# Performance work log

Measured on AMD Instinct MI355X. Metric: run time of the kernel, lower is better.

Reference implementation:

```python
import jax, jax.numpy as jnp
from jax import lax
import numpy as np

EPS = 1e-5

def _conv(x, w, pad):
    return lax.conv_general_dilated(x, w, (1, 1), ((pad, pad), (pad, pad)),
                                    dimension_numbers=('NCHW', 'OIHW', 'NCHW'))

def _bn_relu(x, g, b, m, v):
    scale = g * lax.rsqrt(v + EPS)
    shift = b - m * scale
    return jax.nn.relu(x * scale[:, None, None] + shift[:, None, None])

def _pam(x, kw, kb, vw, vb, gamma):
    # x: [B,C,H,W]; key/query share the same 1x1 conv (as in source)
    B, C, H, W = x.shape
    q = (_conv(x, kw, 0) + kb[:, None, None]).reshape(B, -1, H * W)      # [B,C/8,HW]
    attn = jax.nn.softmax(jnp.einsum('bci,bcj->bij', q, q), axis=-1)     # [B,HW,HW]
    v = (_conv(x, vw, 0) + vb[:, None, None]).reshape(B, C, H * W)       # [B,C,HW]
    out = jnp.einsum('bcj,bij->bci', v, attn).reshape(B, C, H, W)        # value @ attn^T
    return gamma * out + x

def _cam(x, gamma):
    B, C, H, W = x.shape
    f = x.reshape(B, C, H * W)
    energy = jnp.einsum('bcm,bdm->bcd', f, f)                            # [B,C,C]
    attn = jax.nn.softmax(jnp.max(energy, -1, keepdims=True) - energy, axis=-1)
    out = jnp.einsum('bcd,bdm->bcm', attn, f).reshape(B, C, H, W)
    return gamma * out + x

def setup_inputs() -> dict:
    key = jax.random.key(0)
    ks = iter(jax.random.split(key, 40))
    Cin, Cm, Cout = 512, 128, 64  # in_channels, in_channels//ratio, out_channels
    Ck = Cm // 8                  # PAM key channels
    n = lambda shape, s: jax.random.normal(next(ks), shape, jnp.float32) * s
    def bn(c):
        return dict(g=n((c,), 1.0) * 0 + 1.0 + n((c,), 0.1),
                    b=n((c,), 0.1), m=n((c,), 0.1), v=jnp.abs(n((c,), 0.5)) + 0.5)
    bn11, bn12, bn21, bn22 = bn(Cm), bn(Cm), bn(Cm), bn(Cm)
    return {
        'x': jax.random.normal(next(ks), (4, Cin, 64, 64), jnp.float32),
        'w11': n((Cm, Cin, 3, 3), 0.02), 'g11': bn11['g'], 'b11': bn11['b'], 'm11': bn11['m'], 'v11': bn11['v'],
        'w12': n((Cm, Cin, 3, 3), 0.02), 'g12': bn12['g'], 'b12': bn12['b'], 'm12': bn12['m'], 'v12': bn12['v'],
        'pam_kw': n((Ck, Cm, 1, 1), 0.05), 'pam_kb': n((Ck,), 0.02),
        'pam_vw': n((Cm, Cm, 1, 1), 0.05), 'pam_vb': n((Cm,), 0.02),
        'pam_gamma': n((1,), 0.1), 'cam_gamma': n((1,), 0.1),
        'w21': n((Cm, Cm, 3, 3), 0.03), 'g21': bn21['g'], 'b21': bn21['b'], 'm21': bn21['m'], 'v21': bn21['v'],
        'w22': n((Cm, Cm, 3, 3), 0.03), 'g22': bn22['g'], 'b22': bn22['b'], 'm22': bn22['m'], 'v22': bn22['v'],
        'w31': n((Cout, Cm, 1, 1), 0.05), 'b31': n((Cout,), 0.02),
        'w32': n((Cout, Cm, 1, 1), 0.05), 'b32': n((Cout,), 0.02),
        'w4':  n((Cout, Cm, 1, 1), 0.05), 'b4':  n((Cout,), 0.02),
    }

def reference(x, w11, g11, b11, m11, v11, w12, g12, b12, m12, v12,
              pam_kw, pam_kb, pam_vw, pam_vb, pam_gamma, cam_gamma,
              w21, g21, b21, m21, v21, w22, g22, b22, m22, v22,
              w31, b31, w32, b32, w4, b4):
    # Dropout2d(p=0.1) is identity at eval time; BatchNorm uses running stats.
    feat1 = _bn_relu(_conv(x, w11, 1), g11, b11, m11, v11)
    pa_feat = _pam(feat1, pam_kw, pam_kb, pam_vw, pam_vb, pam_gamma)
    pa_conv = _bn_relu(_conv(pa_feat, w21, 1), g21, b21, m21, v21)
    pa_out = _conv(pa_conv, w31, 0) + b31[:, None, None]

    feat2 = _bn_relu(_conv(x, w12, 1), g12, b12, m12, v12)
    ca_feat = _cam(feat2, cam_gamma)
    ca_conv = _bn_relu(_conv(ca_feat, w22, 1), g22, b22, m22, v22)
    ca_out = _conv(ca_conv, w32, 0) + b32[:, None, None]

    feat_sum = pa_conv + ca_conv
    feat_sum_out = _conv(feat_sum, w4, 0) + b4[:, None, None]
    return jnp.stack([pa_out, ca_out, feat_sum_out])  # [3,B,Cout,H,W]
```

## Files before the change

kernel.cpp:

```cpp
#include <hip/hip_runtime.h>
#include <stdint.h>

typedef unsigned short u16;
typedef unsigned int   u32;
typedef unsigned long long u64;
typedef __attribute__((ext_vector_type(8))) short bf16x8;
typedef __attribute__((ext_vector_type(4))) float f32x4;

#define DEV static __device__ __forceinline__

DEV float b2f(u16 u){ u32 x = ((u32)u) << 16; float f; __builtin_memcpy(&f, &x, 4); return f; }
DEV u16 f2b(float f){ u32 x; __builtin_memcpy(&x, &f, 4); return (u16)((x + 0x7fffu + ((x >> 16) & 1u)) >> 16); }
DEV u16 f2b_trunc(float f){ u32 x; __builtin_memcpy(&x, &f, 4); return (u16)(x >> 16); }
DEV float ldf(const void* p, int i, int flg){
  return flg ? b2f(((const u16*)p)[i]) : ((const float*)p)[i];
}
DEV void gload_lds16(const u16* g, u16* l){
  __builtin_amdgcn_global_load_lds((const __attribute__((address_space(1))) void*)g,
                                   (__attribute__((address_space(3))) void*)l, 16, 0, 0);
}

static constexpr int HW   = 4096;
static constexpr int PPIX = 4356;

__global__ void k_prep(
    const u32* __restrict__ x,
    const void* g0,const void* b0,const void* m0,const void* v0,
    const void* g1,const void* b1,const void* m1,const void* v1,
    const void* g2,const void* b2,const void* m2,const void* v2,
    const void* g3,const void* b3,const void* m3,const void* v3,
    int* __restrict__ flag, float* scale, float* shift)
{
  __shared__ int cnt;
  __shared__ int sflag;
  const int t = threadIdx.x;
  if (t == 0) cnt = 0;
  __syncthreads();
  const u32 w  = x[t];
  const u32 eb = (w >> 7) & 0xFFu;
  if (eb >= 100u && eb <= 150u) atomicAdd(&cnt, 1);
  __syncthreads();
  if (t == 0){ sflag = (cnt > 384) ? 1 : 0; *flag = sflag; }
  __syncthreads();
  const int flg = sflag;
  const int set = t >> 7, c = t & 127;
  const void *gp,*bp,*mp,*vp;
  if      (set == 0){gp=g0;bp=b0;mp=m0;vp=v0;}
  else if (set == 1){gp=g1;bp=b1;mp=m1;vp=v1;}
  else if (set == 2){gp=g2;bp=b2;mp=m2;vp=v2;}
  else              {gp=g3;bp=b3;mp=m3;vp=v3;}
  const float sc = ldf(gp,c,flg) * rsqrtf(ldf(vp,c,flg) + 1e-5f);
  scale[t] = sc;
  shift[t] = ldf(bp,c,flg) - ldf(mp,c,flg) * sc;
}

__global__ void k_cvt5(
    const void* s0,const void* s1,const void* s2,const void* s3,const void* s4,
    const int* __restrict__ flagp,
    u16* d0,u16* d1,u16* d2,u16* d3,u16* d4)
{
  const int g = blockIdx.x * 256 + threadIdx.x;
  if (g >= 10752) return;
  const void* s; u16* d; int base;
  if      (g < 512) { s=s0; d=d0; base=0;    }
  else if (g < 4608){ s=s1; d=d1; base=512;  }
  else if (g < 6656){ s=s2; d=d2; base=4608; }
  else if (g < 8704){ s=s3; d=d3; base=6656; }
  else              { s=s4; d=d4; base=8704; }
  const int i = g - base;
  u64 ov;
  if (*flagp){
    ov = ((const u64*)s)[i];
  } else {
    const float4 f = ((const float4*)s)[i];
    const u16 a0 = f2b(f.x), a1 = f2b(f.y), a2 = f2b(f.z), a3 = f2b(f.w);
    ov = (u64)a0 | ((u64)a1 << 16) | ((u64)a2 << 32) | ((u64)a3 << 48);
  }
  ((u64*)d)[i] = ov;
}

__global__ void k_reorder4(
    const void* w11,const void* w12,const void* w21,const void* w22,
    const int* __restrict__ flagp,
    u16* o11,u16* o12,u16* o21,u16* o22)
{
  int blk = blockIdx.x;
  const void* win; u16* wout; int cin;
  if      (blk < 2304){ win=w11; wout=o11; cin=512; }
  else if (blk < 4608){ win=w12; wout=o12; cin=512; blk-=2304; }
  else if (blk < 5184){ win=w21; wout=o21; cin=128; blk-=4608; }
  else                { win=w22; wout=o22; cin=128; blk-=5184; }
  const int idx = blk * 256 + threadIdx.x;
  const int flg = *flagp;
  const int n9 = cin * 9;
  const int co = idx / n9;
  const int rem = idx - co * n9;
  const int ci = rem / 9;
  const int rs = rem - ci * 9;
  const u16 v = flg ? ((const u16*)win)[idx] : f2b(((const float*)win)[idx]);
  wout[co * n9 + rs * cin + ci] = v;
}

__global__ void k_halo3(u16* __restrict__ xT, u16* __restrict__ f1, u16* __restrict__ cf)
{
  int blk = blockIdx.x;
  u16* buf; int cmask, csh;
  if      (blk < 260){ buf = xT; cmask = 511; csh = 9; }
  else if (blk < 325){ buf = f1; cmask = 127; csh = 7; blk -= 260; }
  else               { buf = cf; cmask = 127; csh = 7; blk -= 325; }
  const int tid = blk * 256 + threadIdx.x;
  const int e  = tid * 8;
  const int cc = e & cmask;
  const int rem = e >> csh;
  const int hp = rem % 260;
  const int b  = rem / 260;
  int pix;
  if      (hp < 66)  pix = hp;
  else if (hp < 132) pix = 65 * 66 + (hp - 66);
  else if (hp < 196) pix = (hp - 132 + 1) * 66;
  else               pix = (hp - 196 + 1) * 66 + 65;
  uint4 z; z.x = 0; z.y = 0; z.z = 0; z.w = 0;
  *(uint4*)(buf + ((size_t)b * PPIX + pix) * (cmask + 1) + cc) = z;
}

__global__ __launch_bounds__(256) void k_xT(
    const void* __restrict__ src, const int* __restrict__ flagp, u16* __restrict__ dst)
{
  const int t = threadIdx.x, wave = t >> 6, lane = t & 63;
  const int pb = blockIdx.x & 31, ct = (blockIdx.x >> 5) & 7, b = blockIdx.x >> 8;
  const int c  = ct * 64 + lane;
  const int p0 = pb * 128 + wave * 32;
  const size_t sbase = ((size_t)(b * 512) + c) * 4096 + p0;

  u16 vals[32];
  if (*flagp){
    const u16* s = (const u16*)src + sbase;
    #pragma unroll
    for (int k = 0; k < 4; ++k){
      uint4 v = *(const uint4*)(s + k * 8);
      __builtin_memcpy(&vals[k * 8], &v, 16);
    }
  } else {
    const float* s = (const float*)src + sbase;
    #pragma unroll
    for (int k = 0; k < 8; ++k){
      float4 v = *(const float4*)(s + k * 4);
      vals[k*4+0] = f2b(v.x); vals[k*4+1] = f2b(v.y);
      vals[k*4+2] = f2b(v.z); vals[k*4+3] = f2b(v.w);
    }
  }
  const int hrow = (p0 >> 6) * 66 + (p0 & 63) + 67;
  u16* d = dst + ((size_t)b * PPIX + hrow) * 512 + c;
  #pragma unroll
  for (int k = 0; k < 32; ++k) d[(size_t)k * 512] = vals[k];
}

template<int CIN_, bool PADOUT_, bool DUALB_>
__global__ __launch_bounds__(256) void k_cgemm(
    const u16* __restrict__ xA, const u16* __restrict__ xB,
    const u16* __restrict__ wA, const u16* __restrict__ wB,
    const float* __restrict__ scale, const float* __restrict__ shift,
    u16* __restrict__ outA, u16* __restrict__ outBp, u16* __restrict__ outB2)
{
  constexpr int K9   = 9 * CIN_;
  constexpr int NCH  = CIN_ / 64;
  constexpr int OPIX = PADOUT_ ? PPIX : 4096;

  __shared__ __align__(16) u16 At[128 * 64];
  __shared__ __align__(16) u16 Bt[64 * 64];

  const int t = threadIdx.x;
  const int w = t >> 6, lane = t & 63;
  const int l16 = lane & 15, quad = lane >> 4;

  const int cid = blockIdx.x >> 8;
  const int rem = blockIdx.x & 255;
  const int b   = rem >> 6;
  const int p0  = (rem & 63) << 6;

  const u16* xin = cid ? xB : xA;
  const u16* wK  = cid ? wB : wA;
  const float* sc = scale + cid * 128;
  const float* sh = shift + cid * 128;

  const int rowS = t >> 3;
  const int sw   = ((t & 7) ^ (rowS & 7)) << 3;

  const u16* gA[4]; u16* lA[4];
  #pragma unroll
  for (int k = 0; k < 4; ++k){
    gA[k] = wK + (size_t)(k * 32 + rowS) * K9 + sw;
    lA[k] = At + k * 2048 + w * 512;
  }
  const u16* gB[2]; u16* lB[2];
  #pragma unroll
  for (int k = 0; k < 2; ++k){
    const int px = p0 + k * 32 + rowS;
    const int h = px >> 6, wc = px & 63;
    gB[k] = xin + ((size_t)b * PPIX + h * 66 + wc) * CIN_ + sw;
    lB[k] = Bt + k * 2048 + w * 512;
  }

  f32x4 acc[4][2];
  #pragma unroll
  for (int mi = 0; mi < 4; ++mi)
    #pragma unroll
    for (int ni = 0; ni < 2; ++ni){
      acc[mi][ni][0]=0.f; acc[mi][ni][1]=0.f; acc[mi][ni][2]=0.f; acc[mi][ni][3]=0.f;
    }

  const int wc4 = (w >> 1) << 6;
  const int wp4 = (w & 1) << 5;

  #pragma unroll 1
  for (int tap = 0; tap < 9; ++tap){
    const int tb = (tap / 3) * 66 + (tap % 3);
    #pragma unroll 1
    for (int cc = 0; cc < NCH; ++cc){
      const int offA = tap * CIN_ + cc * 64;
      const int offB = tb  * CIN_ + cc * 64;
      #pragma unroll
      for (int k = 0; k < 4; ++k) gload_lds16(gA[k] + offA, lA[k]);
      #pragma unroll
      for (int k = 0; k < 2; ++k) gload_lds16(gB[k] + offB, lB[k]);
      __syncthreads();
      #pragma unroll
      for (int ks = 0; ks < 2; ++ks){
        bf16x8 af[4], bf[2];
        const int col = ((ks * 4 + quad) ^ (l16 & 7)) << 3;
        #pragma unroll
        for (int mi = 0; mi < 4; ++mi)
          af[mi] = *(const bf16x8*)(At + ((wc4 + mi * 16 + l16) << 6) + col);
        #pragma unroll
        for (int ni = 0; ni < 2; ++ni)
          bf[ni] = *(const bf16x8*)(Bt + ((wp4 + ni * 16 + l16) << 6) + col);
        #pragma unroll
        for (int mi = 0; mi < 4; ++mi)
          #pragma unroll
          for (int ni = 0; ni < 2; ++ni)
            acc[mi][ni] = __builtin_amdgcn_mfma_f32_16x16x32_bf16(af[mi], bf[ni], acc[mi][ni], 0, 0, 0);
      }
      __syncthreads();
    }
  }

  u16* outp = cid ? outBp : outA;
  #pragma unroll
  for (int mi = 0; mi < 4; ++mi){
    #pragma unroll
    for (int ni = 0; ni < 2; ++ni){
      const int px = p0 + wp4 + ni * 16 + l16;
      const int opix = PADOUT_ ? ((px >> 6) * 66 + (px & 63) + 67) : px;
      const int co4 = wc4 + mi * 16 + quad * 4;
      u16 pk[4];
      #pragma unroll
      for (int rr = 0; rr < 4; ++rr)
        pk[rr] = f2b(fmaxf(acc[mi][ni][rr] * sc[co4 + rr] + sh[co4 + rr], 0.f));
      u64 pkv; __builtin_memcpy(&pkv, pk, 8);
      *(u64*)(outp + ((size_t)b * OPIX + opix) * 128 + co4) = pkv;
      if constexpr (DUALB_){
        if (cid){
          #pragma unroll
          for (int rr = 0; rr < 4; ++rr)
            outB2[((size_t)(b * 128) + co4 + rr) * 4096 + px] = pk[rr];
        }
      }
    }
  }
}

template<int CIN_, int CO_, int EPI_, bool SUM2_, bool PADIN_, bool PADOUT_, bool WPB_>
__global__ __launch_bounds__(256) void k_convT(
    const u16* __restrict__ xin, const u16* __restrict__ xin2,
    const u16* __restrict__ wK,
    const void* __restrict__ bias, const int* __restrict__ flagp,
    u16* __restrict__ outB, float* __restrict__ outF)
{
  constexpr int K    = CIN_;
  constexpr int MT   = CO_ / 16;
  constexpr int IPIX = PADIN_ ? PPIX : 4096;
  constexpr int OPIX = PADOUT_ ? PPIX : 4096;

  const int tid  = threadIdx.x;
  const int wave = tid >> 6;
  const int lane = tid & 63;
  const int l16  = lane & 15;
  const int quad = lane >> 4;

  int tile = blockIdx.x * 4 + wave;
  const int nt = tile & 255; tile >>= 8;
  const int mt = tile % MT;
  const int b  = tile / MT;

  const int p = nt * 16 + l16;
  const int h = p >> 6, wc = p & 63;

  const u16* wrow = wK + (WPB_ ? (size_t)b * CO_ * K : 0)
                       + (size_t)(mt * 16 + l16) * K + quad * 8;
  const u16* xb   = xin + (size_t)b * IPIX * CIN_ + quad * 8;

  f32x4 acc = {0.f, 0.f, 0.f, 0.f};

  const int poff = PADIN_ ? (h * 66 + wc + 67) : p;
  const u16* xrs = xb + (size_t)poff * CIN_;
  const u16* xrs2 = nullptr;
  if constexpr (SUM2_) xrs2 = xin2 + (size_t)b * IPIX * CIN_ + quad * 8 + (size_t)poff * CIN_;
  #pragma unroll
  for (int ci0 = 0; ci0 < CIN_; ci0 += 32){
    bf16x8 af = *(const bf16x8*)(wrow + ci0);
    bf16x8 bf;
    if constexpr (SUM2_){
      bf16x8 b1 = *(const bf16x8*)(xrs + ci0);
      bf16x8 b2 = *(const bf16x8*)(xrs2 + ci0);
      #pragma unroll
      for (int j = 0; j < 8; ++j)
        bf[j] = (short)f2b(b2f((u16)b1[j]) + b2f((u16)b2[j]));
    } else {
      bf = *(const bf16x8*)(xrs + ci0);
    }
    acc = __builtin_amdgcn_mfma_f32_16x16x32_bf16(af, bf, acc, 0, 0, 0);
  }

  const int flg = *flagp;

  if constexpr (EPI_ == 4){
    #pragma unroll
    for (int rr = 0; rr < 4; ++rr){
      const int co = quad * 4 + rr;
      const float vv = acc[rr] + ldf(bias, co, flg);
      const u16 hb = f2b(vv);
      const float lo = vv - b2f(hb);
      const size_t qaddr = ((size_t)b * 4096 + p) * 16 + co;
      outB[qaddr] = hb;
      ((u16*)outF)[qaddr] = f2b(lo);
    }
  } else if constexpr (EPI_ == 5){
    const int js = p >> 10, chv = (p >> 6) & 15, ksv = (p >> 5) & 1;
    const int qd = (p >> 3) & 3, jj = p & 7;
    #pragma unroll
    for (int rr = 0; rr < 4; ++rr){
      const int lc = quad * 4 + rr;
      const float vv = acc[rr] + ldf(bias, mt * 16 + lc, flg);
      const size_t addr = ((size_t)((b * 4 + js) * 16 + chv)) * 8192
                        + (size_t)((((mt * 2 + ksv) * 64) + qd * 16 + lc) * 8 + jj);
      outB[addr] = f2b(vv);
    }
  } else if constexpr (EPI_ == 6){
    const float g = ldf(bias, 0, flg);
    const int opix = PADOUT_ ? (h * 66 + wc + 67) : p;
    const int co4 = mt * 16 + quad * 4;
    const size_t addr = ((size_t)b * OPIX + opix) * CO_ + co4;
    u64 rv = *(const u64*)(xin2 + (size_t)b * OPIX * CO_ + (size_t)opix * CO_ + co4);
    u16 rk[4]; __builtin_memcpy(rk, &rv, 8);
    u16 pk[4];
    #pragma unroll
    for (int rr = 0; rr < 4; ++rr)
      pk[rr] = f2b(g * acc[rr] + b2f(rk[rr]));
    u64 pkv; __builtin_memcpy(&pkv, pk, 8);
    *(u64*)(outB + addr) = pkv;
  } else {
    #pragma unroll
    for (int rr = 0; rr < 4; ++rr){
      const int co = mt * 16 + quad * 4 + rr;
      const float vv = acc[rr] + ldf(bias, co, flg);
      const size_t addr = ((size_t)(b * CO_) + co) * 4096 + p;
      if constexpr (EPI_ == 2) outB[addr] = f2b(vv);
      else { if (flg) outB[addr] = f2b(vv); else outF[addr] = vv; }
    }
  }
}

__global__ __launch_bounds__(256) void k_pam_flash(
    const u16* __restrict__ qTh, const u16* __restrict__ qTl,
    const u16* __restrict__ vt,
    u16* __restrict__ po, float* __restrict__ pm, float* __restrict__ pl)
{
  __shared__ __align__(16) u16 vls[2][1024 * 8];
  __shared__ __align__(16) u16 pls[4][128 * 8];

  const int t    = threadIdx.x;
  const int wave = t >> 6, lane = t & 63;
  const int l16  = lane & 15, quad = lane >> 4;

  const int bid = blockIdx.x;
  const int js  = bid & 3, it = (bid >> 2) & 63, b = bid >> 8;
  const int i0  = it * 64;
  const int jbase = js * 1024;

  const u16* qTbh = qTh + ((size_t)b * 4096) * 16;
  const u16* qTbl = qTl + ((size_t)b * 4096) * 16;

  bf16x8 af_hl, af_h0 = {};
  {
    const int i = i0 + wave * 16 + l16;
    const u16* src = ((quad < 2) ? qTbh : qTbl) + (size_t)i * 16 + (quad & 1) * 8;
    *(uint4*)&af_hl = *(const uint4*)src;
    if (quad < 2) af_h0 = af_hl;
  }

  const u16* vsrc = vt + ((size_t)(b * 4 + js) * 16) * 8192 + (size_t)t * 8;
  int vdstO[4];
  #pragma unroll
  for (int k = 0; k < 4; ++k) vdstO[k] = (wave * 64 + 256 * k) * 8;

  #pragma unroll
  for (int k = 0; k < 4; ++k)
    gload_lds16(vsrc + (size_t)k * 2048, &vls[0][0] + vdstO[k]);

  float mloc[4] = {-3e38f, -3e38f, -3e38f, -3e38f};
  #pragma unroll 1
  for (int ch = 0; ch < 16; ++ch){
    #pragma unroll
    for (int ns = 0; ns < 4; ++ns){
      const int j = jbase + ch * 64 + ns * 16 + l16;
      bf16x8 bh;
      *(uint4*)&bh = *(const uint4*)(qTbh + (size_t)j * 16 + (quad & 1) * 8);
      f32x4 z = {0.f, 0.f, 0.f, 0.f};
      z = __builtin_amdgcn_mfma_f32_16x16x32_bf16(af_hl, bh, z, 0, 0, 0);
      #pragma unroll
      for (int r = 0; r < 4; ++r) mloc[r] = fmaxf(mloc[r], z[r]);
    }
  }
  float mrow[4];
  #pragma unroll
  for (int r = 0; r < 4; ++r){
    float mm = mloc[r];
    mm = fmaxf(mm, __shfl_xor(mm, 1));
    mm = fmaxf(mm, __shfl_xor(mm, 2));
    mm = fmaxf(mm, __shfl_xor(mm, 4));
    mm = fmaxf(mm, __shfl_xor(mm, 8));
    mrow[r] = mm;
  }

  const short oneb = (short)0x3F80;
  const bf16x8 vones = {oneb,oneb,oneb,oneb,oneb,oneb,oneb,oneb};

  f32x4 oacc[8];
  #pragma unroll
  for (int cs = 0; cs < 8; ++cs){ oacc[cs][0]=0.f; oacc[cs][1]=0.f; oacc[cs][2]=0.f; oacc[cs][3]=0.f; }
  f32x4 lacc = {0.f, 0.f, 0.f, 0.f};

  #pragma unroll 1
  for (int ch = 0; ch < 16; ++ch){
    const int j0 = ch * 64;
    const int cur = ch & 1;
    __syncthreads();

    if (ch < 15){
      u16* nbuf = &vls[cur ^ 1][0];
      const u16* nsrc = vsrc + (size_t)(ch + 1) * 8192;
      #pragma unroll
      for (int k = 0; k < 4; ++k)
        gload_lds16(nsrc + (size_t)k * 2048, nbuf + vdstO[k]);
    }

    #pragma unroll
    for (int ns = 0; ns < 4; ++ns){
      const int j = jbase + j0 + ns * 16 + l16;
      bf16x8 bh, bl;
      *(uint4*)&bh = *(const uint4*)(qTbh + (size_t)j * 16 + (quad & 1) * 8);
      *(uint4*)&bl = *(const uint4*)(qTbl + (size_t)j * 16 + (quad & 1) * 8);
      f32x4 z = {0.f, 0.f, 0.f, 0.f};
      z = __builtin_amdgcn_mfma_f32_16x16x32_bf16(af_hl, bh, z, 0, 0, 0);
      z = __builtin_amdgcn_mfma_f32_16x16x32_bf16(af_h0, bl, z, 0, 0, 0);
      const int ks = ns >> 1;
      const int qp = (ns * 2 + (l16 >> 3)) & 3;
      #pragma unroll
      for (int r = 0; r < 4; ++r){
        const float p = __expf(z[r] - mrow[r]);
        pls[wave][(ks * 64 + qp * 16 + quad * 4 + r) * 8 + (l16 & 7)] = f2b_trunc(p);
      }
    }

    const u16* vcur = &vls[cur][0];
    #pragma unroll
    for (int ks = 0; ks < 2; ++ks){
      bf16x8 pf = *(const bf16x8*)(pls[wave] + ((ks * 64 + lane) << 3));
      #pragma unroll
      for (int cs = 0; cs < 8; ++cs){
        bf16x8 vf = *(const bf16x8*)(vcur + (((cs * 2 + ks) * 64 + lane) << 3));
        oacc[cs] = __builtin_amdgcn_mfma_f32_16x16x32_bf16(pf, vf, oacc[cs], 0, 0, 0);
      }
      lacc = __builtin_amdgcn_mfma_f32_16x16x32_bf16(pf, vones, lacc, 0, 0, 0);
    }
  }

  u16* pob = po + (size_t)bid * 64 * 128;
  #pragma unroll
  for (int cs = 0; cs < 8; ++cs)
    #pragma unroll
    for (int r = 0; r < 4; ++r)
      pob[(wave * 16 + quad * 4 + r) * 128 + cs * 16 + l16] = f2b(oacc[cs][r]);
  if (l16 == 0){
    #pragma unroll
    for (int r = 0; r < 4; ++r){
      pm[(size_t)bid * 64 + wave * 16 + quad * 4 + r] = mrow[r];
      pl[(size_t)bid * 64 + wave * 16 + quad * 4 + r] = lacc[r];
    }
  }
}

__global__ __launch_bounds__(256) void k_pam_comb2(
    const u16* __restrict__ po, const float* __restrict__ pm, const float* __restrict__ pl,
    const void* __restrict__ gptr, const int* __restrict__ flagp,
    u16* __restrict__ featT)
{
  __shared__ float wgt[4][64];
  const int t  = threadIdx.x;
  const int it = blockIdx.x & 63, b = blockIdx.x >> 6;
  const int base = (b * 64 + it) * 4;
  if (t < 64){
    const float m0 = pm[(size_t)(base+0)*64 + t];
    const float m1 = pm[(size_t)(base+1)*64 + t];
    const float m2 = pm[(size_t)(base+2)*64 + t];
    const float m3 = pm[(size_t)(base+3)*64 + t];
    const float M  = fmaxf(fmaxf(m0, m1), fmaxf(m2, m3));
    const float e0 = __expf(m0 - M), e1 = __expf(m1 - M);
    const float e2 = __expf(m2 - M), e3 = __expf(m3 - M);
    const float L  = pl[(size_t)(base+0)*64+t]*e0 + pl[(size_t)(base+1)*64+t]*e1
                   + pl[(size_t)(base+2)*64+t]*e2 + pl[(size_t)(base+3)*64+t]*e3;
    const float li = 1.0f / L;
    wgt[0][t] = e0*li; wgt[1][t] = e1*li; wgt[2][t] = e2*li; wgt[3][t] = e3*li;
  }
  __syncthreads();
  const float g = ldf(gptr, 0, *flagp);
  const int c = t & 127, ih = t >> 7;
  const int i0 = it * 64;
  for (int st = 0; st < 32; ++st){
    const int il = ih + st * 2;
    float acc = 0.f;
    #pragma unroll
    for (int s = 0; s < 4; ++s)
      acc += wgt[s][il] * b2f(po[((size_t)(base+s)*64 + il)*128 + c]);
    const int i = i0 + il;
    const int pix = (i >> 6) * 66 + (i & 63) + 67;
    u16* addr = featT + ((size_t)b * PPIX + pix) * 128 + c;
    *addr = f2b(g * acc + b2f(*addr));
  }
}

__global__ __launch_bounds__(256) void k_cam_energy(
    const u16* __restrict__ f, u16* __restrict__ attnc)
{
  __shared__ float els[16][132];
  const int t = threadIdx.x, wave = t >> 6, lane = t & 63;
  const int l16 = lane & 15, quad = lane >> 4;
  const int ct = blockIdx.x & 7, b = blockIdx.x >> 3;
  const u16* fb = f + (size_t)b * 128 * 4096;
  const int c0 = ct * 16;
  const int d0 = wave * 32;

  f32x4 e0 = {0.f,0.f,0.f,0.f}, e1 = {0.f,0.f,0.f,0.f};
  #pragma unroll 2
  for (int k0 = 0; k0 < 4096; k0 += 32){
    bf16x8 afr, bf0, bf1;
    *(uint4*)&afr = *(const uint4*)(fb + (size_t)(c0 + l16) * 4096 + k0 + quad * 8);
    *(uint4*)&bf0 = *(const uint4*)(fb + (size_t)(d0 + l16) * 4096 + k0 + quad * 8);
    *(uint4*)&bf1 = *(const uint4*)(fb + (size_t)(d0 + 16 + l16) * 4096 + k0 + quad * 8);
    e0 = __builtin_amdgcn_mfma_f32_16x16x32_bf16(afr, bf0, e0, 0, 0, 0);
    e1 = __builtin_amdgcn_mfma_f32_16x16x32_bf16(afr, bf1, e1, 0, 0, 0);
  }
  #pragma unroll
  for (int r = 0; r < 4; ++r){
    els[quad * 4 + r][d0 + l16]      = e0[r];
    els[quad * 4 + r][d0 + 16 + l16] = e1[r];
  }
  __syncthreads();
  const int c = wave * 4 + quad, sg = l16;
  float mn = 3e38f;
  float ev[8];
  #pragma unroll
  for (int k = 0; k < 8; ++k){ ev[k] = els[c][sg * 8 + k]; mn = fminf(mn, ev[k]); }
  mn = fminf(mn, __shfl_xor(mn, 1));
  mn = fminf(mn, __shfl_xor(mn, 2));
  mn = fminf(mn, __shfl_xor(mn, 4));
  mn = fminf(mn, __shfl_xor(mn, 8));
  float s = 0.f;
  #pragma unroll
  for (int k = 0; k < 8; ++k){ ev[k] = __expf(mn - ev[k]); s += ev[k]; }
  s += __shfl_xor(s, 1); s += __shfl_xor(s, 2);
  s += __shfl_xor(s, 4); s += __shfl_xor(s, 8);
  const float inv = 1.0f / s;
  u16* dst = attnc + ((size_t)b * 128 + c0 + c) * 128 + sg * 8;
  #pragma unroll
  for (int k = 0; k < 8; ++k) dst[k] = f2b(ev[k] * inv);
}

extern "C" void kernel_launch(void* const* d_in, const int* in_sizes, int n_in,
                              void* d_out, int out_size, void* d_ws, size_t ws_size,
                              hipStream_t stream)
{
  (void)in_sizes; (void)n_in; (void)out_size; (void)ws_size;

  const void* x    = d_in[0];
  const void* w11  = d_in[1];
  const void* g11  = d_in[2];
  const void* b11  = d_in[3];
  const void* m11  = d_in[4];
  const void* v11  = d_in[5];
  const void* w12  = d_in[6];
  const void* g12  = d_in[7];
  const void* b12  = d_in[8];
  const void* m12  = d_in[9];
  const void* v12  = d_in[10];
  const void* kw   = d_in[11];
  const void* kb   = d_in[12];
  const void* vw   = d_in[13];
  const void* vb   = d_in[14];
  const void* pgam = d_in[15];
  const void* cgam = d_in[16];
  const void* w21  = d_in[17];
  const void* g21  = d_in[18];
  const void* b21  = d_in[19];
  const void* m21  = d_in[20];
  const void* v21  = d_in[21];
  const void* w22  = d_in[22];
  const void* g22  = d_in[23];
  const void* b22  = d_in[24];
  const void* m22  = d_in[25];
  const void* v22  = d_in[26];
  const void* w31  = d_in[27];
  const void* b31  = d_in[28];
  const void* w32  = d_in[29];
  const void* b32  = d_in[30];
  const void* w4   = d_in[31];
  const void* b4   = d_in[32];

  char* wsb = (char*)d_ws;
  size_t off = 0;
  auto alloc = [&](size_t bytes) -> void* {
    void* pp = wsb + off;
    off += (bytes + 255) & ~(size_t)255;
    return pp;
  };
  u16*   xT      = (u16*)alloc((size_t)4 * PPIX * 512 * 2);
  u16*   feat1T  = (u16*)alloc((size_t)4 * PPIX * 128 * 2);
  u16*   feat2T  = (u16*)alloc((size_t)4 * PPIX * 128 * 2);
  u16*   feat2cm = (u16*)alloc((size_t)4 * 128 * HW * 2);
  u16*   cafeatT = (u16*)alloc((size_t)4 * PPIX * 128 * 2);
  u16*   vbuf    = (u16*)alloc((size_t)4 * 128 * HW * 2);
  u16*   caconvT = (u16*)alloc((size_t)4 * HW * 128 * 2);
  u16*   qTh     = (u16*)alloc((size_t)4 * HW * 16 * 2);
  u16*   qTl     = (u16*)alloc((size_t)4 * HW * 16 * 2);
  float* pm      = (float*)alloc((size_t)1024 * 64 * 4);
  float* pl      = (float*)alloc((size_t)1024 * 64 * 4);
  u16*   attnc   = (u16*)alloc((size_t)4 * 128 * 128 * 2);
  float* scale   = (float*)alloc(512 * 4);
  float* shift   = (float*)alloc(512 * 4);
  u16*   w11r    = (u16*)alloc((size_t)128 * 4608 * 2);
  u16*   w12r    = (u16*)alloc((size_t)128 * 4608 * 2);
  u16*   w21r    = (u16*)alloc((size_t)128 * 1152 * 2);
  u16*   w22r    = (u16*)alloc((size_t)128 * 1152 * 2);
  u16*   kwb     = (u16*)alloc((size_t)16 * 128 * 2);
  u16*   vwb     = (u16*)alloc((size_t)128 * 128 * 2);
  u16*   w31b    = (u16*)alloc((size_t)64 * 128 * 2);
  u16*   w32b    = (u16*)alloc((size_t)64 * 128 * 2);
  u16*   w4b     = (u16*)alloc((size_t)64 * 128 * 2);
  int*   flag    = (int*)alloc(256);
  u16*   po      = xT;

  k_prep<<<1, 512, 0, stream>>>((const u32*)x,
                                g11,b11,m11,v11, g12,b12,m12,v12,
                                g21,b21,m21,v21, g22,b22,m22,v22, flag, scale, shift);
  k_halo3<<<390, 256, 0, stream>>>(xT, feat1T, cafeatT);
  k_xT<<<1024, 256, 0, stream>>>(x, flag, xT);
  k_reorder4<<<5760, 256, 0, stream>>>(w11, w12, w21, w22, flag, w11r, w12r, w21r, w22r);
  k_cvt5<<<42, 256, 0, stream>>>(kw, vw, w31, w32, w4, flag, kwb, vwb, w31b, w32b, w4b);

  k_cgemm<512, true, true><<<512, 256, 0, stream>>>(
      xT, xT, w11r, w12r, scale, shift, feat1T, feat2T, feat2cm);

  k_convT<128,16,4,false,true,false,false><<<256,256,0,stream>>>(
      feat1T, nullptr, kwb, kb, flag, qTh, (float*)qTl);
  k_convT<128,128,5,false,true,false,false><<<2048,256,0,stream>>>(
      feat1T, nullptr, vwb, vb, flag, vbuf, nullptr);
  k_pam_flash<<<1024, 256, 0, stream>>>(qTh, qTl, vbuf, po, pm, pl);
  k_pam_comb2<<<256, 256, 0, stream>>>(po, pm, pl, pgam, flag, feat1T);

  k_cam_energy<<<32, 256, 0, stream>>>(feat2cm, attnc);
  k_convT<128,128,6,false,true,true,true><<<2048,256,0,stream>>>(
      feat2T, feat2T, attnc, cgam, flag, cafeatT, nullptr);

  k_cgemm<128, false, false><<<512, 256, 0, stream>>>(
      feat1T, cafeatT, w21r, w22r, scale + 256, shift + 256, vbuf, caconvT, nullptr);

  const size_t SEC = (size_t)4 * 64 * HW;
  u16*   outB = (u16*)d_out;
  float* outF = (float*)d_out;
  k_convT<128,64,3,false,false,false,false><<<1024,256,0,stream>>>(
      vbuf,    nullptr, w31b, b31, flag, outB,           outF);
  k_convT<128,64,3,false,false,false,false><<<1024,256,0,stream>>>(
      caconvT, nullptr, w32b, b32, flag, outB + SEC,     outF + SEC);
  k_convT<128,64,3,true ,false,false,false><<<1024,256,0,stream>>>(
      vbuf,    caconvT, w4b,  b4,  flag, outB + 2 * SEC, outF + 2 * SEC);
}
```

Before: 386.5 us.

## Double-buffer LDS tiles in conv GEMM and interleave block index mapping

Replaces the single-buffered tap/channel loop in the 3x3 conv GEMM kernel with a flattened loop over two LDS buffers. The next tile's global-to-LDS loads are issued before the MFMA work on the current tile, with one barrier per iteration instead of two, so load latency can overlap compute. It also remaps blockIdx so the branch id and batch index vary fastest, which changes which blocks share weights and pixel rows in cache at the same time. LDS use per block doubles, which can lower occupancy, and the overlap depends on the compiler not inserting waits on the async LDS loads before the shared-memory reads.

```diff
diff --git a/kernel.cpp b/kernel.cpp
--- a/kernel.cpp
+++ b/kernel.cpp
@@ -164,19 +164,19 @@
 {
   constexpr int K9   = 9 * CIN_;
   constexpr int NCH  = CIN_ / 64;
+  constexpr int NIT  = 9 * NCH;
   constexpr int OPIX = PADOUT_ ? PPIX : 4096;
 
-  __shared__ __align__(16) u16 At[128 * 64];
-  __shared__ __align__(16) u16 Bt[64 * 64];
+  __shared__ __align__(16) u16 At[2][128 * 64];
+  __shared__ __align__(16) u16 Bt[2][64 * 64];
 
   const int t = threadIdx.x;
   const int w = t >> 6, lane = t & 63;
   const int l16 = lane & 15, quad = lane >> 4;
 
-  const int cid = blockIdx.x >> 8;
-  const int rem = blockIdx.x & 255;
-  const int b   = rem >> 6;
-  const int p0  = (rem & 63) << 6;
+  const int cid = (blockIdx.x >> 2) & 1;
+  const int b   = blockIdx.x & 3;
+  const int p0  = (blockIdx.x >> 3) << 6;
 
   const u16* xin = cid ? xB : xA;
   const u16* wK  = cid ? wB : wA;
@@ -186,20 +186,32 @@
   const int rowS = t >> 3;
   const int sw   = ((t & 7) ^ (rowS & 7)) << 3;
 
-  const u16* gA[4]; u16* lA[4];
-  #pragma unroll
-  for (int k = 0; k < 4; ++k){
+  const u16* gA[4];
+  #pragma unroll
+  for (int k = 0; k < 4; ++k)
     gA[k] = wK + (size_t)(k * 32 + rowS) * K9 + sw;
-    lA[k] = At + k * 2048 + w * 512;
-  }
-  const u16* gB[2]; u16* lB[2];
+  const u16* gB[2];
   #pragma unroll
   for (int k = 0; k < 2; ++k){
     const int px = p0 + k * 32 + rowS;
     const int h = px >> 6, wc = px & 63;
     gB[k] = xin + ((size_t)b * PPIX + h * 66 + wc) * CIN_ + sw;
-    lB[k] = Bt + k * 2048 + w * 512;
-  }
+  }
+  const int ldst = w * 512;
+
+  auto stage = [&](int it, int buf){
+    const int tap = it / NCH;
+    const int cc  = it - tap * NCH;
+    const int offA = it * 64;
+    const int tb   = (tap / 3) * 66 + (tap % 3);
+    const int offB = tb * CIN_ + cc * 64;
+    #pragma unroll
+    for (int k = 0; k < 4; ++k)
+      gload_lds16(gA[k] + offA, &At[buf][0] + k * 2048 + ldst);
+    #pragma unroll
+    for (int k = 0; k < 2; ++k)
+      gload_lds16(gB[k] + offB, &Bt[buf][0] + k * 2048 + ldst);
+  };
 
   f32x4 acc[4][2];
   #pragma unroll
@@ -212,35 +224,31 @@
   const int wc4 = (w >> 1) << 6;
   const int wp4 = (w & 1) << 5;
 
+  stage(0, 0);
+
   #pragma unroll 1
-  for (int tap = 0; tap < 9; ++tap){
-    const int tb = (tap / 3) * 66 + (tap % 3);
-    #pragma unroll 1
-    for (int cc = 0; cc < NCH; ++cc){
-      const int offA = tap * CIN_ + cc * 64;
-      const int offB = tb  * CIN_ + cc * 64;
-      #pragma unroll
-      for (int k = 0; k < 4; ++k) gload_lds16(gA[k] + offA, lA[k]);
-      #pragma unroll
-      for (int k = 0; k < 2; ++k) gload_lds16(gB[k] + offB, lB[k]);
-      __syncthreads();
-      #pragma unroll
-      for (int ks = 0; ks < 2; ++ks){
-        bf16x8 af[4], bf[2];
-        const int col = ((ks * 4 + quad) ^ (l16 & 7)) << 3;
-        #pragma unroll
-        for (int mi = 0; mi < 4; ++mi)
-          af[mi] = *(const bf16x8*)(At + ((wc4 + mi * 16 + l16) << 6) + col);
+  for (int it = 0; it < NIT; ++it){
+    const int cur = it & 1;
+    __syncthreads();
+    if (it + 1 < NIT) stage(it + 1, cur ^ 1);
+
+    const u16* Ab = &At[cur][0];
+    const u16* Bb = &Bt[cur][0];
+    #pragma unroll
+    for (int ks = 0; ks < 2; ++ks){
+      bf16x8 af[4], bf[2];
+      const int col = ((ks * 4 + quad) ^ (l16 & 7)) << 3;
+      #pragma unroll
+      for (int mi = 0; mi < 4; ++mi)
+        af[mi] = *(const bf16x8*)(Ab + ((wc4 + mi * 16 + l16) << 6) + col);
+      #pragma unroll
+      for (int ni = 0; ni < 2; ++ni)
+        bf[ni] = *(const bf16x8*)(Bb + ((wp4 + ni * 16 + l16) << 6) + col);
+      #pragma unroll
+      for (int mi = 0; mi < 4; ++mi)
         #pragma unroll
         for (int ni = 0; ni < 2; ++ni)
-          bf[ni] = *(const bf16x8*)(Bt + ((wp4 + ni * 16 + l16) << 6) + col);
-        #pragma unroll
-        for (int mi = 0; mi < 4; ++mi)
-          #pragma unroll
-          for (int ni = 0; ni < 2; ++ni)
-            acc[mi][ni] = __builtin_amdgcn_mfma_f32_16x16x32_bf16(af[mi], bf[ni], acc[mi][ni], 0, 0, 0);
-      }
-      __syncthreads();
+          acc[mi][ni] = __builtin_amdgcn_mfma_f32_16x16x32_bf16(af[mi], bf[ni], acc[mi][ni], 0, 0, 0);
     }
   }
 
```

Measured after the change: 390.8 us. Within noise of the previous version (+1.1%).
